# Performance work log

Measured on AMD Instinct MI355X. Metric: run time of the kernel, lower is better.

Reference implementation:

```python
import jax, jax.numpy as jnp
import numpy as np

B, K, D_APP, D_K, D_G = 8, 512, 768, 96, 96

def setup_inputs() -> dict:
    key = jax.random.key(0)
    ks = jax.random.split(key, 10)
    s = 0.02
    return {
        "f_a": jax.random.normal(ks[0], (B, K, D_APP), dtype=jnp.float32),
        "position_embedding": jax.random.uniform(ks[1], (B, K, K, D_G), dtype=jnp.float32),
        "WG_w": jax.random.normal(ks[2], (1, D_G), dtype=jnp.float32) * s,
        "WG_b": jnp.zeros((1,), dtype=jnp.float32),
        "WK_w": jax.random.normal(ks[3], (D_K, D_APP), dtype=jnp.float32) * s,
        "WK_b": jnp.zeros((D_K,), dtype=jnp.float32),
        "WQ_w": jax.random.normal(ks[4], (D_K, D_APP), dtype=jnp.float32) * s,
        "WQ_b": jnp.zeros((D_K,), dtype=jnp.float32),
        "WV_w": jax.random.normal(ks[5], (D_K, D_APP), dtype=jnp.float32) * s,
        "WV_b": jnp.zeros((D_K,), dtype=jnp.float32),
    }

def reference(f_a, position_embedding, WG_w, WG_b, WK_w, WK_b, WQ_w, WQ_b, WV_w, WV_b):
    # geometric gate: [B,K,K,geo] -> [B,K,K]
    w_g = jax.nn.relu(jnp.einsum('bmng,og->bmno', position_embedding, WG_w) + WG_b)[..., 0]
    w_k = f_a @ WK_w.T + WK_b  # [B,K,dk], index m (keys)
    w_q = f_a @ WQ_w.T + WQ_b  # [B,K,dk], index n (queries)
    scaled_dot = jnp.einsum('bmd,bnd->bmn', w_k, w_q) / np.sqrt(D_K).astype(np.float32)
    logits = jnp.log(jnp.clip(w_g, 1e-6)) + scaled_dot  # [B,m,n]
    attn = jax.nn.softmax(logits, axis=1)  # softmax over m (dim=1 in torch)
    w_v = f_a @ WV_w.T + WV_b  # [B,K,dk]
    out = jnp.einsum('bmn,bmd->bnd', attn, w_v)  # sum over m -> [B,K,dk]
    return out
```

## Files before the change

kernel.cpp:

```cpp
#include <hip/hip_runtime.h>
#include <cstdint>

#define B_   8
#define K_   512
#define DAPP 768
#define DK   96
#define DG   96

#define P_F ((size_t)B_ * K_ * DK)
#define LG_OFF (3 * P_F)

__device__ __forceinline__ float dot4(float4 a, float4 b) {
    return a.x * b.x + a.y * b.y + a.z * b.z + a.w * b.w;
}

__global__ __launch_bounds__(256) void proj_kernel(
    const float* __restrict__ fa,
    const float* __restrict__ WK, const float* __restrict__ WKb,
    const float* __restrict__ WQ, const float* __restrict__ WQb,
    const float* __restrict__ WV, const float* __restrict__ WVb,
    float* __restrict__ ws) {
    const int mat = blockIdx.y;
    const float* W  = (mat == 0) ? WK  : (mat == 1) ? WQ  : WV;
    const float* Wb = (mat == 0) ? WKb : (mat == 1) ? WQb : WVb;
    float* outp = ws + (size_t)mat * P_F;

    const int t  = threadIdx.x;
    const int tr = t >> 4;
    const int tc = t & 15;
    const int row = blockIdx.x * 16 + tr;

    const float4* fa4 = (const float4*)fa + (size_t)row * (DAPP / 4);
    const float4* W4  = (const float4*)W;

    float acc[6] = {0.f, 0.f, 0.f, 0.f, 0.f, 0.f};
    const float4* wrow[6];
#pragma unroll
    for (int j = 0; j < 6; ++j)
        wrow[j] = W4 + (size_t)(tc + 16 * j) * (DAPP / 4);

#pragma unroll 2
    for (int q = 0; q < DAPP / 4; ++q) {
        float4 a = fa4[q];
#pragma unroll
        for (int j = 0; j < 6; ++j)
            acc[j] += dot4(a, wrow[j][q]);
    }
#pragma unroll
    for (int j = 0; j < 6; ++j) {
        int c = tc + 16 * j;
        outp[(size_t)row * DK + c] = acc[j] + Wb[c];
    }
}

__global__ __launch_bounds__(256) void logits_kernel(
    const float* __restrict__ pe,
    const float* __restrict__ WGw, const float* __restrict__ WGb,
    float* ws) {
    const int bm = blockIdx.x;
    const int b  = bm >> 9;

    const int t = threadIdx.x;
    const int p = t & 7;
    const int nidx = t >> 3;

    const float4* wk4 = (const float4*)ws + (size_t)bm * 24;
    const float4* wq4 = (const float4*)(ws + P_F);
    const float4* wg4 = (const float4*)WGw;
    const float4* pe4 = (const float4*)pe + (size_t)bm * K_ * 24;
    float* lg = ws + LG_OFF + (size_t)bm * K_;

    float4 kf0 = wk4[p], kf1 = wk4[p + 8], kf2 = wk4[p + 16];
    float4 gf0 = wg4[p], gf1 = wg4[p + 8], gf2 = wg4[p + 16];
    const float gb = WGb[0];
    const float inv_sqrt_dk = 0.10206207f;

    for (int it = 0; it < 16; ++it) {
        const int n = it * 32 + nidx;
        const float4* pr = pe4 + (size_t)n * 24 + p;
        float s1 = dot4(pr[0], gf0) + dot4(pr[8], gf1) + dot4(pr[16], gf2);
        const float4* qr = wq4 + ((size_t)(b * K_ + n)) * 24 + p;
        float s2 = dot4(qr[0], kf0) + dot4(qr[8], kf1) + dot4(qr[16], kf2);
        s1 += __shfl_xor(s1, 1); s2 += __shfl_xor(s2, 1);
        s1 += __shfl_xor(s1, 2); s2 += __shfl_xor(s2, 2);
        s1 += __shfl_xor(s1, 4); s2 += __shfl_xor(s2, 4);
        if (p == 0) {
            float gate = fmaxf(s1 + gb, 1e-6f);
            lg[n] = __logf(gate) + s2 * inv_sqrt_dk;
        }
    }
}

__global__ __launch_bounds__(384) void softmax_pv_kernel(
    const float* __restrict__ ws_c, float* __restrict__ out) {
    __shared__ __align__(16) float sp[512 * 20];
    const int blk = blockIdx.x;
    const int b = blk >> 5;
    const int n0 = (blk & 31) * 16;
    const int t = threadIdx.x;

    const float* logits = ws_c + LG_OFF + (size_t)b * K_ * K_;
    const float4* lg4 = (const float4*)logits;

    for (int i = t; i < 2048; i += 384) {
        int mrow = i >> 2, q = i & 3;
        float4 v = lg4[(size_t)mrow * (K_ / 4) + (n0 >> 2) + q];
        *(float4*)&sp[mrow * 20 + q * 4] = v;
    }
    __syncthreads();

    if (t < 256) {
        const int c = t >> 4, l = t & 15;
        float vals[32];
        float mx = -1e30f;
#pragma unroll
        for (int i = 0; i < 32; ++i) {
            vals[i] = sp[(i * 16 + l) * 20 + c];
            mx = fmaxf(mx, vals[i]);
        }
        mx = fmaxf(mx, __shfl_xor(mx, 8));
        mx = fmaxf(mx, __shfl_xor(mx, 4));
        mx = fmaxf(mx, __shfl_xor(mx, 2));
        mx = fmaxf(mx, __shfl_xor(mx, 1));
        float sum = 0.f;
#pragma unroll
        for (int i = 0; i < 32; ++i) {
            float e = __expf(vals[i] - mx);
            vals[i] = e;
            sum += e;
        }
        sum += __shfl_xor(sum, 8);
        sum += __shfl_xor(sum, 4);
        sum += __shfl_xor(sum, 2);
        sum += __shfl_xor(sum, 1);
        float inv = 1.f / sum;
#pragma unroll
        for (int i = 0; i < 32; ++i)
            sp[(i * 16 + l) * 20 + c] = vals[i] * inv;
    }
    __syncthreads();

    const int d = t % 96;
    const int g = t / 96;
    const float* wv = ws_c + 2 * P_F + (size_t)b * K_ * DK;
    float a0 = 0.f, a1 = 0.f, a2 = 0.f, a3 = 0.f;
#pragma unroll 8
    for (int mrow = 0; mrow < 512; ++mrow) {
        float v = wv[(size_t)mrow * DK + d];
        float4 p4 = *(const float4*)&sp[mrow * 20 + g * 4];
        a0 += p4.x * v; a1 += p4.y * v; a2 += p4.z * v; a3 += p4.w * v;
    }
    const int nbase = n0 + g * 4;
    float* ob = out + ((size_t)b * K_ + nbase) * DK + d;
    ob[0]      = a0;
    ob[DK]     = a1;
    ob[2 * DK] = a2;
    ob[3 * DK] = a3;
}

extern "C" void kernel_launch(void* const* d_in, const int* in_sizes, int n_in,
                              void* d_out, int out_size, void* d_ws, size_t ws_size,
                              hipStream_t stream) {
    (void)in_sizes; (void)n_in; (void)out_size; (void)ws_size;
    const float* fa  = (const float*)d_in[0];
    const float* pe  = (const float*)d_in[1];
    const float* WGw = (const float*)d_in[2];
    const float* WGb = (const float*)d_in[3];
    const float* WKw = (const float*)d_in[4];
    const float* WKb = (const float*)d_in[5];
    const float* WQw = (const float*)d_in[6];
    const float* WQb = (const float*)d_in[7];
    const float* WVw = (const float*)d_in[8];
    const float* WVb = (const float*)d_in[9];
    float* out = (float*)d_out;
    float* ws  = (float*)d_ws;

    proj_kernel<<<dim3(256, 3), 256, 0, stream>>>(fa, WKw, WKb, WQw, WQb, WVw, WVb, ws);
    logits_kernel<<<B_ * K_, 256, 0, stream>>>(pe, WGw, WGb, ws);
    softmax_pv_kernel<<<B_ * 32, 384, 0, stream>>>(ws, out);
}
```

Baseline: 608.4 us.

## Fuse geometric gate, online softmax and PV into split-m flash kernel with combine

Result: slower. 643.6 us (+5.8%).

```diff
diff --git a/kernel.cpp b/kernel.cpp
--- a/kernel.cpp
+++ b/kernel.cpp
@@ -5,10 +5,15 @@
 #define K_   512
 #define DAPP 768
 #define DK   96
-#define DG   96
-
-#define P_F ((size_t)B_ * K_ * DK)
-#define LG_OFF (3 * P_F)
+#define NT   16
+#define MT   32
+#define MS   8
+#define MCH  (K_ / MS)
+#define P_F  ((size_t)B_ * K_ * DK)
+#define SD_OFF (3 * P_F)
+#define SD_SZ  ((size_t)B_ * K_ * K_)
+#define PART_OFF (SD_OFF + SD_SZ)
+#define PART_STRIDE 1568
 
 __device__ __forceinline__ float dot4(float4 a, float4 b) {
     return a.x * b.x + a.y * b.y + a.z * b.z + a.w * b.w;
@@ -23,6 +28,7 @@
     const int mat = blockIdx.y;
     const float* W  = (mat == 0) ? WK  : (mat == 1) ? WQ  : WV;
     const float* Wb = (mat == 0) ? WKb : (mat == 1) ? WQb : WVb;
+    const float scale = (mat == 0) ? 0.10206207f : 1.0f;
     float* outp = ws + (size_t)mat * P_F;
 
     const int t  = threadIdx.x;
@@ -49,113 +55,206 @@
 #pragma unroll
     for (int j = 0; j < 6; ++j) {
         int c = tc + 16 * j;
-        outp[(size_t)row * DK + c] = acc[j] + Wb[c];
-    }
-}
-
-__global__ __launch_bounds__(256) void logits_kernel(
-    const float* __restrict__ pe,
-    const float* __restrict__ WGw, const float* __restrict__ WGb,
-    float* ws) {
+        outp[(size_t)row * DK + c] = (acc[j] + Wb[c]) * scale;
+    }
+}
+
+__global__ __launch_bounds__(256) void sd_kernel(
+    const float* __restrict__ wk, const float* __restrict__ wq,
+    float* __restrict__ sd) {
     const int bm = blockIdx.x;
     const int b  = bm >> 9;
-
     const int t = threadIdx.x;
     const int p = t & 7;
     const int nidx = t >> 3;
 
-    const float4* wk4 = (const float4*)ws + (size_t)bm * 24;
-    const float4* wq4 = (const float4*)(ws + P_F);
-    const float4* wg4 = (const float4*)WGw;
-    const float4* pe4 = (const float4*)pe + (size_t)bm * K_ * 24;
-    float* lg = ws + LG_OFF + (size_t)bm * K_;
-
+    const float4* wk4 = (const float4*)wk + (size_t)bm * 24;
+    const float4* wq4 = (const float4*)wq;
     float4 kf0 = wk4[p], kf1 = wk4[p + 8], kf2 = wk4[p + 16];
-    float4 gf0 = wg4[p], gf1 = wg4[p + 8], gf2 = wg4[p + 16];
-    const float gb = WGb[0];
-    const float inv_sqrt_dk = 0.10206207f;
-
+    float* sdr = sd + (size_t)bm * K_;
+
+#pragma unroll 2
     for (int it = 0; it < 16; ++it) {
         const int n = it * 32 + nidx;
-        const float4* pr = pe4 + (size_t)n * 24 + p;
-        float s1 = dot4(pr[0], gf0) + dot4(pr[8], gf1) + dot4(pr[16], gf2);
         const float4* qr = wq4 + ((size_t)(b * K_ + n)) * 24 + p;
-        float s2 = dot4(qr[0], kf0) + dot4(qr[8], kf1) + dot4(qr[16], kf2);
-        s1 += __shfl_xor(s1, 1); s2 += __shfl_xor(s2, 1);
-        s1 += __shfl_xor(s1, 2); s2 += __shfl_xor(s2, 2);
-        s1 += __shfl_xor(s1, 4); s2 += __shfl_xor(s2, 4);
-        if (p == 0) {
-            float gate = fmaxf(s1 + gb, 1e-6f);
-            lg[n] = __logf(gate) + s2 * inv_sqrt_dk;
+        float s = dot4(qr[0], kf0) + dot4(qr[8], kf1) + dot4(qr[16], kf2);
+        s += __shfl_xor(s, 1);
+        s += __shfl_xor(s, 2);
+        s += __shfl_xor(s, 4);
+        if (p == 0) sdr[n] = s;
+    }
+}
+
+__global__ __launch_bounds__(256) void flash_kernel(
+    const float* __restrict__ pe,
+    const float* __restrict__ WGw, const float* __restrict__ WGb,
+    const float* __restrict__ ws_base,
+    float* __restrict__ parts) {
+    __shared__ float lt[MT][NT + 1];
+    __shared__ __align__(16) float wvl[MT][DK];
+    __shared__ float s_m[NT], s_l[NT], s_scale[NT];
+
+    const int bid = blockIdx.x;
+    const int nt = bid & 31;
+    const int ms = (bid >> 5) & 7;
+    const int b  = bid >> 8;
+    const int n0 = nt * NT;
+    const int m0 = ms * MCH;
+    const int t = threadIdx.x;
+
+    const int p = t & 3;
+    const int pairn = (t >> 2) & 15;
+    const int pairm = t >> 6;
+
+    const int cn = t / 12;
+    const int co = t % 12;
+
+    int smi[3], sf[3];
+#pragma unroll
+    for (int r = 0; r < 3; ++r) {
+        int idx = t + 256 * r;
+        smi[r] = idx / 24;
+        sf[r]  = idx % 24;
+    }
+
+    const float4* wg4 = (const float4*)WGw;
+    float4 gf[6];
+#pragma unroll
+    for (int j = 0; j < 6; ++j) gf[j] = wg4[p + 4 * j];
+    const float gb = WGb[0];
+
+    if (t < NT) { s_m[t] = -1e30f; s_l[t] = 0.f; }
+
+    const float4* pe4 = (const float4*)pe;
+    const float*  sd  = ws_base + SD_OFF;
+    const float4* wv4 = (const float4*)(ws_base + 2 * P_F);
+
+    float4 accA = {0.f, 0.f, 0.f, 0.f};
+    float4 accB = {0.f, 0.f, 0.f, 0.f};
+
+    for (int tile = 0; tile < MCH / MT; ++tile) {
+        const int mb = m0 + tile * MT;
+
+#pragma unroll
+        for (int r = 0; r < 3; ++r)
+            ((float4*)wvl)[t + 256 * r] =
+                wv4[((size_t)(b * K_ + mb + smi[r])) * 24 + sf[r]];
+
+#pragma unroll 2
+        for (int pass = 0; pass < 8; ++pass) {
+            const int mi = pass * 4 + pairm;
+            const int m  = mb + mi;
+            const float4* pr =
+                pe4 + ((size_t)((b * K_ + m) * K_ + n0 + pairn)) * 24 + p;
+            float s = dot4(pr[0],  gf[0]) + dot4(pr[4],  gf[1]) +
+                      dot4(pr[8],  gf[2]) + dot4(pr[12], gf[3]) +
+                      dot4(pr[16], gf[4]) + dot4(pr[20], gf[5]);
+            s += __shfl_xor(s, 1);
+            s += __shfl_xor(s, 2);
+            if (p == 0) {
+                float sdv = sd[(size_t)((b * K_ + m) * K_) + n0 + pairn];
+                lt[mi][pairn] = __logf(fmaxf(s + gb, 1e-6f)) + sdv;
+            }
         }
-    }
-}
-
-__global__ __launch_bounds__(384) void softmax_pv_kernel(
-    const float* __restrict__ ws_c, float* __restrict__ out) {
-    __shared__ __align__(16) float sp[512 * 20];
-    const int blk = blockIdx.x;
-    const int b = blk >> 5;
-    const int n0 = (blk & 31) * 16;
+        __syncthreads();
+
+        {
+            const int n = t >> 4, l = t & 15;
+            float v0 = lt[l][n], v1 = lt[l + 16][n];
+            float tmax = fmaxf(v0, v1);
+            tmax = fmaxf(tmax, __shfl_xor(tmax, 1));
+            tmax = fmaxf(tmax, __shfl_xor(tmax, 2));
+            tmax = fmaxf(tmax, __shfl_xor(tmax, 4));
+            tmax = fmaxf(tmax, __shfl_xor(tmax, 8));
+            float mold = s_m[n];
+            float mnew = fmaxf(mold, tmax);
+            float e0 = __expf(v0 - mnew), e1 = __expf(v1 - mnew);
+            float ts = e0 + e1;
+            ts += __shfl_xor(ts, 1);
+            ts += __shfl_xor(ts, 2);
+            ts += __shfl_xor(ts, 4);
+            ts += __shfl_xor(ts, 8);
+            float sc = __expf(mold - mnew);
+            if (l == 0) {
+                s_m[n] = mnew;
+                s_l[n] = s_l[n] * sc + ts;
+                s_scale[n] = sc;
+            }
+            lt[l][n] = e0;
+            lt[l + 16][n] = e1;
+        }
+        __syncthreads();
+
+        if (t < 192) {
+            float sc = s_scale[cn];
+            accA.x *= sc; accA.y *= sc; accA.z *= sc; accA.w *= sc;
+            accB.x *= sc; accB.y *= sc; accB.z *= sc; accB.w *= sc;
+#pragma unroll 8
+            for (int mi = 0; mi < MT; ++mi) {
+                float pv = lt[mi][cn];
+                float4 wA = *(const float4*)&wvl[mi][co * 8];
+                float4 wB = *(const float4*)&wvl[mi][co * 8 + 4];
+                accA.x = fmaf(pv, wA.x, accA.x);
+                accA.y = fmaf(pv, wA.y, accA.y);
+                accA.z = fmaf(pv, wA.z, accA.z);
+                accA.w = fmaf(pv, wA.w, accA.w);
+                accB.x = fmaf(pv, wB.x, accB.x);
+                accB.y = fmaf(pv, wB.y, accB.y);
+                accB.z = fmaf(pv, wB.z, accB.z);
+                accB.w = fmaf(pv, wB.w, accB.w);
+            }
+        }
+        __syncthreads();
+    }
+
+    float* pp = parts + (size_t)bid * PART_STRIDE;
+    if (t < 192) {
+        *(float4*)&pp[cn * DK + co * 8]     = accA;
+        *(float4*)&pp[cn * DK + co * 8 + 4] = accB;
+    }
+    if (t >= 192 && t < 192 + NT) {
+        int n = t - 192;
+        pp[1536 + n] = s_m[n];
+        pp[1552 + n] = s_l[n];
+    }
+}
+
+__global__ __launch_bounds__(192) void combine_kernel(
+    const float* __restrict__ parts, float* __restrict__ out) {
+    const int bid = blockIdx.x;
+    const int nt = bid & 31, b = bid >> 5;
     const int t = threadIdx.x;
-
-    const float* logits = ws_c + LG_OFF + (size_t)b * K_ * K_;
-    const float4* lg4 = (const float4*)logits;
-
-    for (int i = t; i < 2048; i += 384) {
-        int mrow = i >> 2, q = i & 3;
-        float4 v = lg4[(size_t)mrow * (K_ / 4) + (n0 >> 2) + q];
-        *(float4*)&sp[mrow * 20 + q * 4] = v;
-    }
-    __syncthreads();
-
-    if (t < 256) {
-        const int c = t >> 4, l = t & 15;
-        float vals[32];
-        float mx = -1e30f;
-#pragma unroll
-        for (int i = 0; i < 32; ++i) {
-            vals[i] = sp[(i * 16 + l) * 20 + c];
-            mx = fmaxf(mx, vals[i]);
-        }
-        mx = fmaxf(mx, __shfl_xor(mx, 8));
-        mx = fmaxf(mx, __shfl_xor(mx, 4));
-        mx = fmaxf(mx, __shfl_xor(mx, 2));
-        mx = fmaxf(mx, __shfl_xor(mx, 1));
-        float sum = 0.f;
-#pragma unroll
-        for (int i = 0; i < 32; ++i) {
-            float e = __expf(vals[i] - mx);
-            vals[i] = e;
-            sum += e;
-        }
-        sum += __shfl_xor(sum, 8);
-        sum += __shfl_xor(sum, 4);
-        sum += __shfl_xor(sum, 2);
-        sum += __shfl_xor(sum, 1);
-        float inv = 1.f / sum;
-#pragma unroll
-        for (int i = 0; i < 32; ++i)
-            sp[(i * 16 + l) * 20 + c] = vals[i] * inv;
-    }
-    __syncthreads();
-
-    const int d = t % 96;
-    const int g = t / 96;
-    const float* wv = ws_c + 2 * P_F + (size_t)b * K_ * DK;
-    float a0 = 0.f, a1 = 0.f, a2 = 0.f, a3 = 0.f;
-#pragma unroll 8
-    for (int mrow = 0; mrow < 512; ++mrow) {
-        float v = wv[(size_t)mrow * DK + d];
-        float4 p4 = *(const float4*)&sp[mrow * 20 + g * 4];
-        a0 += p4.x * v; a1 += p4.y * v; a2 += p4.z * v; a3 += p4.w * v;
-    }
-    const int nbase = n0 + g * 4;
-    float* ob = out + ((size_t)b * K_ + nbase) * DK + d;
-    ob[0]      = a0;
-    ob[DK]     = a1;
-    ob[2 * DK] = a2;
-    ob[3 * DK] = a3;
+    const int cn = t / 12, co = t % 12;
+
+    float mv[MS];
+    float M = -1e30f;
+#pragma unroll
+    for (int s = 0; s < MS; ++s) {
+        size_t pidx = (size_t)((b * MS + s) * 32 + nt) * PART_STRIDE;
+        mv[s] = parts[pidx + 1536 + cn];
+        M = fmaxf(M, mv[s]);
+    }
+    float L = 0.f;
+    float4 aA = {0.f, 0.f, 0.f, 0.f};
+    float4 aB = {0.f, 0.f, 0.f, 0.f};
+#pragma unroll
+    for (int s = 0; s < MS; ++s) {
+        size_t pidx = (size_t)((b * MS + s) * 32 + nt) * PART_STRIDE;
+        float w = __expf(mv[s] - M);
+        L += parts[pidx + 1552 + cn] * w;
+        float4 xA = *(const float4*)&parts[pidx + cn * DK + co * 8];
+        float4 xB = *(const float4*)&parts[pidx + cn * DK + co * 8 + 4];
+        aA.x = fmaf(w, xA.x, aA.x); aA.y = fmaf(w, xA.y, aA.y);
+        aA.z = fmaf(w, xA.z, aA.z); aA.w = fmaf(w, xA.w, aA.w);
+        aB.x = fmaf(w, xB.x, aB.x); aB.y = fmaf(w, xB.y, aB.y);
+        aB.z = fmaf(w, xB.z, aB.z); aB.w = fmaf(w, xB.w, aB.w);
+    }
+    float inv = 1.f / L;
+    aA.x *= inv; aA.y *= inv; aA.z *= inv; aA.w *= inv;
+    aB.x *= inv; aB.y *= inv; aB.z *= inv; aB.w *= inv;
+    float* ob = out + ((size_t)(b * K_) + nt * NT + cn) * DK + co * 8;
+    *(float4*)&ob[0] = aA;
+    *(float4*)&ob[4] = aB;
 }
 
 extern "C" void kernel_launch(void* const* d_in, const int* in_sizes, int n_in,
@@ -176,6 +275,7 @@
     float* ws  = (float*)d_ws;
 
     proj_kernel<<<dim3(256, 3), 256, 0, stream>>>(fa, WKw, WKb, WQw, WQb, WVw, WVb, ws);
-    logits_kernel<<<B_ * K_, 256, 0, stream>>>(pe, WGw, WGb, ws);
-    softmax_pv_kernel<<<B_ * 32, 384, 0, stream>>>(ws, out);
-}
+    sd_kernel<<<B_ * K_, 256, 0, stream>>>(ws, ws + P_F, ws + SD_OFF);
+    flash_kernel<<<B_ * MS * 32, 256, 0, stream>>>(pe, WGw, WGb, ws, ws + PART_OFF);
+    combine_kernel<<<B_ * 32, 192, 0, stream>>>(ws + PART_OFF, out);
+}
```
